# Optimization experiments

Measured on AMD Instinct MI355X. Metric: run time of the kernel, lower is better.

Reference implementation:

```python
import jax, jax.numpy as jnp
import numpy as np

NEG_SLOPE = 0.2

def _gat_layer(x, src, dst, W, a_src, a_dst, bias, concat):
    # x: [N, F_in]; W: [F_in, H*C]; a_src/a_dst: [H, C]; bias: [H*C] or [C]
    N = x.shape[0]
    H, C = a_src.shape
    h = (x @ W).reshape(N, H, C)                      # node features per head
    e_src = jnp.einsum('nhc,hc->nh', h, a_src)        # [N, H]
    e_dst = jnp.einsum('nhc,hc->nh', h, a_dst)        # [N, H]
    e = jax.nn.leaky_relu(e_src[src] + e_dst[dst], NEG_SLOPE)  # [E, H]
    # segment softmax over incoming edges of each destination node
    m = jax.ops.segment_max(e, dst, num_segments=N)   # [N, H]
    p = jnp.exp(e - m[dst])
    denom = jax.ops.segment_sum(p, dst, num_segments=N)
    alpha = p / denom[dst]                            # [E, H]
    msg = h[src] * alpha[:, :, None]                  # [E, H, C]
    out = jax.ops.segment_sum(msg, dst, num_segments=N)  # [N, H, C]
    if concat:
        out = out.reshape(N, H * C) + bias
    else:
        out = out.mean(axis=1) + bias
    return out, alpha


def setup_inputs() -> dict:
    key = jax.random.key(0)
    ks = jax.random.split(key, 12)
    N, E = 20000, 320000
    F_in, Ch, Co, H = 256, 64, 64, 8
    x = jax.random.normal(ks[0], (N, F_in), dtype=jnp.float32)
    edge_index = jax.random.randint(ks[1], (2, E), 0, N, dtype=jnp.int64)
    s = 0.05
    return {
        'x': x,
        'edge_index': edge_index,
        'W1': jax.random.normal(ks[2], (F_in, H * Ch), dtype=jnp.float32) * s,
        'att_src1': jax.random.normal(ks[3], (H, Ch), dtype=jnp.float32) * s,
        'att_dst1': jax.random.normal(ks[4], (H, Ch), dtype=jnp.float32) * s,
        'b1': jnp.zeros((H * Ch,), dtype=jnp.float32),
        'W2': jax.random.normal(ks[5], (H * Ch, H * Co), dtype=jnp.float32) * s,
        'att_src2': jax.random.normal(ks[6], (H, Co), dtype=jnp.float32) * s,
        'att_dst2': jax.random.normal(ks[7], (H, Co), dtype=jnp.float32) * s,
        'b2': jnp.zeros((Co,), dtype=jnp.float32),
    }


def reference(x, edge_index, W1, att_src1, att_dst1, b1, W2, att_src2, att_dst2, b2):
    N = x.shape[0]
    # PyG GATConv adds self-loops by default
    loop = jnp.arange(N, dtype=edge_index.dtype)
    src = jnp.concatenate([edge_index[0], loop])
    dst = jnp.concatenate([edge_index[1], loop])
    h1, alpha1 = _gat_layer(x, src, dst, W1, att_src1, att_dst1, b1, concat=True)
    h1 = jax.nn.relu(h1)
    h2, alpha2 = _gat_layer(h1, src, dst, W2, att_src2, att_dst2, b2, concat=False)
    return h2, alpha1, alpha2
```

## Files before the change

kernel.cpp:

```cpp
#include <hip/hip_runtime.h>

#define H 8
#define C 64
#define HC 512
#define NEG 0.2f

typedef __attribute__((ext_vector_type(8))) _Float16 half8v;
typedef __attribute__((ext_vector_type(4))) _Float16 half4v;
typedef __attribute__((ext_vector_type(4))) float f32x4;

__device__ __forceinline__ float leaky(float x) { return x > 0.f ? x : NEG * x; }

#define GLOAD_LDS16(gp, lp) \
  __builtin_amdgcn_global_load_lds((const __attribute__((address_space(1))) unsigned int*)(gp), \
                                   (__attribute__((address_space(3))) unsigned int*)(lp), 16, 0, 0)

__global__ void k_degree(const int* __restrict__ ei, int E, int N, int* __restrict__ deg) {
    int e = blockIdx.x * blockDim.x + threadIdx.x;
    int Et = E + N;
    if (e >= Et) return;
    int d = (e < E) ? ei[E + e] : (e - E);
    atomicAdd(&deg[d], 1);
}

__global__ __launch_bounds__(1024) void k_scan(const int* __restrict__ deg, int N, int* __restrict__ row_start) {
    __shared__ int part[1024];
    int t = threadIdx.x;
    int chunk = (N + 1023) >> 10;
    int lo = t * chunk, hi = min(lo + chunk, N);
    int s = 0;
    for (int i = lo; i < hi; ++i) s += deg[i];
    part[t] = s;
    __syncthreads();
    for (int off = 1; off < 1024; off <<= 1) {
        int v = (t >= off) ? part[t - off] : 0;
        __syncthreads();
        part[t] += v;
        __syncthreads();
    }
    int base = (t == 0) ? 0 : part[t - 1];
    for (int i = lo; i < hi; ++i) { row_start[i] = base; base += deg[i]; }
    if (t == 1023) row_start[N] = part[1023];
}

__global__ void k_fill(const int* __restrict__ ei, int E, int N,
                       const int* __restrict__ row_start, int* __restrict__ cursor,
                       int* __restrict__ csr_src, int* __restrict__ csr_eid,
                       int* __restrict__ csr_dst) {
    int e = blockIdx.x * blockDim.x + threadIdx.x;
    int Et = E + N;
    if (e >= Et) return;
    int d, s;
    if (e < E) { s = ei[e]; d = ei[E + e]; } else { s = e - E; d = s; }
    int pos = atomicAdd(&cursor[d], 1);
    int idx = row_start[d] + pos;
    csr_src[idx] = s;
    csr_eid[idx] = e;
    csr_dst[idx] = d;
}

__global__ void k_tofp16(const float* __restrict__ in, _Float16* __restrict__ out, int n4) {
    int i = blockIdx.x * blockDim.x + threadIdx.x;
    if (i >= n4) return;
    float4 v = reinterpret_cast<const float4*>(in)[i];
    half4v h;
    h[0] = (_Float16)v.x; h[1] = (_Float16)v.y;
    h[2] = (_Float16)v.z; h[3] = (_Float16)v.w;
    reinterpret_cast<half4v*>(out)[i] = h;
}

__global__ void k_tsplit(const float* __restrict__ W, _Float16* __restrict__ th,
                         _Float16* __restrict__ tl, int K, int Nc) {
    int idx = blockIdx.x * blockDim.x + threadIdx.x;
    if (idx >= K * Nc) return;
    int c = idx / K, k = idx - c * K;
    float v = W[(long)k * Nc + c];
    _Float16 hh = (_Float16)v;
    th[idx] = hh;
    tl[idx] = (_Float16)(v - (float)hh);
}

__global__ __launch_bounds__(256) void k_gemm_mfma(const _Float16* __restrict__ A,
                                                   const _Float16* __restrict__ Bh,
                                                   const _Float16* __restrict__ Bl,
                                                   _Float16* __restrict__ Cc, int M, int K, int Pb, int Mpad) {
    __shared__ _Float16 lA[8192], lBh[8192], lBl[8192];
    int bid = blockIdx.x;
    int panel = ((bid >> 5) << 3) + (bid & 7);
    int colb  = (bid >> 3) & 3;
    if (panel >= Pb) return;
    int tid = threadIdx.x;
    int w = tid >> 6, lane = tid & 63;
    int wr = w >> 1, wc = w & 1;
    int r0 = panel * 128, c0 = colb * 128;
    f32x4 acc[4][4] = {};
    int frag_off = ((lane >> 4) * 16 + (lane & 15)) * 8;

    int rb0 = tid >> 6, kc0 = (tid >> 4) & 3, r16_0 = tid & 15;
    int rb1 = (256 + tid) >> 6, kc1 = ((256 + tid) >> 4) & 3;
    long gaBase0 = (long)(r0 + rb0 * 16 + r16_0) * K + kc0 * 8;
    long gbBase0 = (long)(c0 + rb0 * 16 + r16_0) * K + kc0 * 8;
    long gaBase1 = (long)(r0 + rb1 * 16 + r16_0) * K + kc1 * 8;
    long gbBase1 = (long)(c0 + rb1 * 16 + r16_0) * K + kc1 * 8;
    int ldst0 = (w * 64) * 8;
    int ldst1 = (256 + w * 64) * 8;

#define STAGE(buf, k0)  do { \
        int off = (buf) * 4096; \
        GLOAD_LDS16(A  + gaBase0 + (k0), lA  + off + ldst0); \
        GLOAD_LDS16(Bh + gbBase0 + (k0), lBh + off + ldst0); \
        GLOAD_LDS16(Bl + gbBase0 + (k0), lBl + off + ldst0); \
        GLOAD_LDS16(A  + gaBase1 + (k0), lA  + off + ldst1); \
        GLOAD_LDS16(Bh + gbBase1 + (k0), lBh + off + ldst1); \
        GLOAD_LDS16(Bl + gbBase1 + (k0), lBl + off + ldst1); \
    } while (0)

    int nk = K >> 5;
    STAGE(0, 0);
    __syncthreads();
    int cur = 0;
    for (int t = 0; t < nk; ++t) {
        if (t + 1 < nk) STAGE(cur ^ 1, (t + 1) * 32);
        int off = cur * 4096;
        half8v fa[4], fbh[4], fbl[4];
        #pragma unroll
        for (int m = 0; m < 4; ++m) {
            int sa = off + (wr * 4 + m) * 512 + frag_off;
            fa[m] = *reinterpret_cast<half8v*>(&lA[sa]);
            int sb = off + (wc * 4 + m) * 512 + frag_off;
            fbh[m] = *reinterpret_cast<half8v*>(&lBh[sb]);
            fbl[m] = *reinterpret_cast<half8v*>(&lBl[sb]);
        }
        #pragma unroll
        for (int m = 0; m < 4; ++m)
            #pragma unroll
            for (int n = 0; n < 4; ++n) {
                acc[m][n] = __builtin_amdgcn_mfma_f32_16x16x32_f16(fa[m], fbh[n], acc[m][n], 0, 0, 0);
                acc[m][n] = __builtin_amdgcn_mfma_f32_16x16x32_f16(fa[m], fbl[n], acc[m][n], 0, 0, 0);
            }
        __syncthreads();
        cur ^= 1;
    }
#undef STAGE

    int head = colb * 2 + wc;
    long hbase = (long)head * Mpad * 64;
    #pragma unroll
    for (int m = 0; m < 4; ++m)
        #pragma unroll
        for (int j = 0; j < 4; ++j) {
            int gr = r0 + wr * 64 + m * 16 + (lane >> 4) * 4 + j;
            if (gr < M) {
                #pragma unroll
                for (int n = 0; n < 4; ++n)
                    Cc[hbase + (long)gr * 64 + n * 16 + (lane & 15)] = (_Float16)acc[m][n][j];
            }
        }
}

__global__ __launch_bounds__(512) void k_edot(const half8v* __restrict__ hp8,
                                              const float* __restrict__ a_src,
                                              const float* __restrict__ a_dst,
                                              float* __restrict__ e_src, float* __restrict__ e_dst,
                                              int N, int Mpad) {
    int h = threadIdx.x >> 6, lane = threadIdx.x & 63;
    int n8 = lane >> 3, cg = lane & 7;
    int n = blockIdx.x * 8 + n8;
    bool valid = (n < N);
    int nc = valid ? n : (N - 1);
    float as[8], ad[8];
    #pragma unroll
    for (int k = 0; k < 8; ++k) {
        as[k] = a_src[h * 64 + cg * 8 + k];
        ad[k] = a_dst[h * 64 + cg * 8 + k];
    }
    half8v hv = hp8[(long)h * Mpad * 8 + (long)nc * 8 + cg];
    float es = 0.f, ed = 0.f;
    #pragma unroll
    for (int k = 0; k < 8; ++k) {
        es = fmaf((float)hv[k], as[k], es);
        ed = fmaf((float)hv[k], ad[k], ed);
    }
    #pragma unroll
    for (int o = 1; o <= 4; o <<= 1) {
        es += __shfl_xor(es, o);
        ed += __shfl_xor(ed, o);
    }
    if (valid && cg == 0) {
        e_src[n * 8 + h] = es;
        e_dst[n * 8 + h] = ed;
    }
}

__global__ __launch_bounds__(512) void k_edge(const float* __restrict__ e_src,
                                              const float* __restrict__ e_dst,
                                              const int* __restrict__ row_start,
                                              const int* __restrict__ csr_src,
                                              float* __restrict__ alp_csr,
                                              float* __restrict__ inv_buf,
                                              int N) {
    int wid = threadIdx.x >> 6, lane = threadIdx.x & 63;
    int g = lane >> 5;
    int eg = (lane >> 3) & 3;
    int h = lane & 7;
    int n = blockIdx.x * 16 + wid * 2 + g;
    bool valid = (n < N);
    int nc = valid ? n : (N - 1);
    int row = row_start[nc];
    int deg = row_start[nc + 1] - row;
    float ed = e_dst[nc * 8 + h];
    int it = (deg + 3) >> 2;
    int itmax = max(it, __shfl_xor(it, 32));
    float psum = 0.f;
    for (int c = 0; c < itmax; ++c) {
        int e0 = c * 4 + eg;
        int idx = row + min(e0, deg - 1);
        int s = csr_src[idx];
        float p = (e0 < deg) ? __expf(leaky(e_src[s * 8 + h] + ed)) : 0.f;
        psum += p;
        if (valid && e0 < deg)
            alp_csr[(long)idx * 8 + h] = p;
    }
    psum += __shfl_xor(psum, 8);
    psum += __shfl_xor(psum, 16);
    float inv = 1.0f / psum;
    if (valid && eg == 0) inv_buf[n * 8 + h] = inv;
}

__global__ void k_alpha(const int* __restrict__ csr_dst, const int* __restrict__ csr_eid,
                        const float* __restrict__ alp_csr, const float* __restrict__ inv_buf,
                        float* __restrict__ alpha, int Et) {
    int idx = blockIdx.x * blockDim.x + threadIdx.x;
    if (idx >= Et) return;
    int d = csr_dst[idx], eid = csr_eid[idx];
    const float4* p4 = reinterpret_cast<const float4*>(alp_csr) + (long)idx * 2;
    const float4* i4 = reinterpret_cast<const float4*>(inv_buf) + (long)d * 2;
    float4 p0 = p4[0], p1 = p4[1], i0 = i4[0], i1 = i4[1];
    float4 r0, r1;
    r0.x = p0.x * i0.x; r0.y = p0.y * i0.y; r0.z = p0.z * i0.z; r0.w = p0.w * i0.w;
    r1.x = p1.x * i1.x; r1.y = p1.y * i1.y; r1.z = p1.z * i1.z; r1.w = p1.w * i1.w;
    float4* o4 = reinterpret_cast<float4*>(alpha) + (long)eid * 2;
    o4[0] = r0;
    o4[1] = r1;
}

__global__ __launch_bounds__(512) void k_gather(const half8v* __restrict__ hp8,
                                                const int* __restrict__ row_start,
                                                const int* __restrict__ csr_src,
                                                const float* __restrict__ alp_csr,
                                                const float* __restrict__ inv_buf,
                                                const float* __restrict__ bias,
                                                _Float16* __restrict__ h1,
                                                _Float16* __restrict__ accq,
                                                int N, int Mpad, int concat) {
    int wid = threadIdx.x >> 6, lane = threadIdx.x & 63;
    int bid = blockIdx.x;
    int h = bid & 7;
    int g = lane >> 5;
    int eg = (lane >> 3) & 3;
    int cg = lane & 7;
    int n = (bid >> 3) * 16 + wid * 2 + g;
    bool valid = (n < N);
    int nc = valid ? n : (N - 1);
    long hoff = (long)h * Mpad * 8;
    int row = row_start[nc];
    int deg = row_start[nc + 1] - row;
    float inv = inv_buf[nc * 8 + h];
    int it = (deg + 7) >> 3;
    int itmax = max(it, __shfl_xor(it, 32));
    float acc[8] = {};
    int idxA = row + min(eg, deg - 1);
    int idxB = row + min(4 + eg, deg - 1);
    int   sA = csr_src[idxA];
    float aA = alp_csr[(long)idxA * 8 + h];
    int   sB = csr_src[idxB];
    float aB = alp_csr[(long)idxB * 8 + h];
    for (int c = 0; c < itmax; ++c) {
        int e0 = c * 8 + eg, e1 = e0 + 4;
        int sA_c = sA, sB_c = sB;
        float aA_c = (e0 < deg) ? aA : 0.f;
        float aB_c = (e1 < deg) ? aB : 0.f;
        if (c + 1 < itmax) {
            int nA = row + min(e0 + 8, deg - 1);
            int nB = row + min(e1 + 8, deg - 1);
            sA = csr_src[nA];
            aA = alp_csr[(long)nA * 8 + h];
            sB = csr_src[nB];
            aB = alp_csr[(long)nB * 8 + h];
        }
        half8v hA = hp8[hoff + (long)sA_c * 8 + cg];
        half8v hB = hp8[hoff + (long)sB_c * 8 + cg];
        #pragma unroll
        for (int k = 0; k < 8; ++k) {
            acc[k] = fmaf((float)hA[k], aA_c, acc[k]);
            acc[k] = fmaf((float)hB[k], aB_c, acc[k]);
        }
    }
    #pragma unroll
    for (int o = 8; o <= 16; o <<= 1)
        #pragma unroll
        for (int k = 0; k < 8; ++k)
            acc[k] += __shfl_xor(acc[k], o);
    if (!valid) return;
    if (eg == 0) {
        if (concat) {
            half8v hh;
            #pragma unroll
            for (int k = 0; k < 8; ++k) {
                float v = fmaf(acc[k], inv, bias[h * 64 + cg * 8 + k]);
                v = v > 0.f ? v : 0.f;
                hh[k] = (_Float16)v;
            }
            reinterpret_cast<half8v*>(h1)[(long)n * 64 + h * 8 + cg] = hh;
        } else {
            half8v hv2;
            #pragma unroll
            for (int k = 0; k < 8; ++k) hv2[k] = (_Float16)(acc[k] * inv);
            reinterpret_cast<half8v*>(accq)[hoff + (long)n * 8 + cg] = hv2;
        }
    }
}

__global__ void k_mean(const _Float16* __restrict__ accq, const float* __restrict__ bias,
                       float* __restrict__ out, int N, int Mpad) {
    int i = blockIdx.x * blockDim.x + threadIdx.x;
    if (i >= N * 8) return;
    int n = i >> 3, cg = i & 7;
    float s[8] = {};
    #pragma unroll
    for (int h = 0; h < 8; ++h) {
        half8v v = reinterpret_cast<const half8v*>(accq)[(long)h * Mpad * 8 + (long)n * 8 + cg];
        #pragma unroll
        for (int k = 0; k < 8; ++k) s[k] += (float)v[k];
    }
    float4 r0, r1;
    r0.x = s[0] * 0.125f + bias[cg * 8 + 0];
    r0.y = s[1] * 0.125f + bias[cg * 8 + 1];
    r0.z = s[2] * 0.125f + bias[cg * 8 + 2];
    r0.w = s[3] * 0.125f + bias[cg * 8 + 3];
    r1.x = s[4] * 0.125f + bias[cg * 8 + 4];
    r1.y = s[5] * 0.125f + bias[cg * 8 + 5];
    r1.z = s[6] * 0.125f + bias[cg * 8 + 6];
    r1.w = s[7] * 0.125f + bias[cg * 8 + 7];
    float4* o4 = reinterpret_cast<float4*>(out + (long)n * 64 + cg * 8);
    o4[0] = r0;
    o4[1] = r1;
}

extern "C" void kernel_launch(void* const* d_in, const int* in_sizes, int n_in,
                              void* d_out, int out_size, void* d_ws, size_t ws_size,
                              hipStream_t stream) {
    const float* x   = (const float*)d_in[0];
    const int*   ei  = (const int*)d_in[1];
    const float* W1  = (const float*)d_in[2];
    const float* as1 = (const float*)d_in[3];
    const float* ad1 = (const float*)d_in[4];
    const float* b1  = (const float*)d_in[5];
    const float* W2  = (const float*)d_in[6];
    const float* as2 = (const float*)d_in[7];
    const float* ad2 = (const float*)d_in[8];
    const float* b2  = (const float*)d_in[9];

    int N  = in_sizes[0] / 256;
    int E  = in_sizes[1] / 2;
    int Et = E + N;
    int K1 = 256;
    int Mb   = (N + 127) / 128;
    int Mpad = Mb * 128;

    float* out    = (float*)d_out;
    float* h2_out = out;
    float* alpha1 = out + (size_t)N * 64;
    float* alpha2 = alpha1 + (size_t)Et * H;

    _Float16* hpre = (_Float16*)d_ws;
    _Float16* h1   = hpre + (size_t)Mpad * HC;
    _Float16* accq = h1 + (size_t)Mpad * HC;
    _Float16* xh   = accq + (size_t)Mpad * HC;
    _Float16* W1th = xh + (size_t)Mpad * K1;
    _Float16* W1tl = W1th + (size_t)HC * K1;
    _Float16* W2th = W1tl + (size_t)HC * K1;
    _Float16* W2tl = W2th + (size_t)HC * HC;
    float* eS     = (float*)(W2tl + (size_t)HC * HC);
    float* eD     = eS + (size_t)N * H;
    float* alpcsr = eD + (size_t)N * H;
    float* invb   = alpcsr + (size_t)Et * H;
    int*   deg    = (int*)(invb + (size_t)N * H);
    int*   cursor = deg + N;
    int*   row_st = cursor + N;
    int*   csr_src= row_st + N + 1;
    int*   csr_eid= csr_src + Et;
    int*   csr_dst= csr_eid + Et;

    hipMemsetAsync(deg, 0, (size_t)2 * N * sizeof(int), stream);
    int tb = 256;
    k_degree<<<(Et + tb - 1) / tb, tb, 0, stream>>>(ei, E, N, deg);
    k_scan<<<1, 1024, 0, stream>>>(deg, N, row_st);
    k_fill<<<(Et + tb - 1) / tb, tb, 0, stream>>>(ei, E, N, row_st, cursor, csr_src, csr_eid, csr_dst);

    int n4 = N * K1 / 4;
    k_tofp16<<<(n4 + tb - 1) / tb, tb, 0, stream>>>(x, xh, n4);
    k_tsplit<<<(K1 * HC + tb - 1) / tb, tb, 0, stream>>>(W1, W1th, W1tl, K1, HC);
    k_tsplit<<<(HC * HC + tb - 1) / tb, tb, 0, stream>>>(W2, W2th, W2tl, HC, HC);

    int Pb8 = ((Mb + 7) / 8) * 8;
    int ggemm = Pb8 * 4;
    int gedot = (N + 7) / 8;
    int gedge = (N + 15) / 16;
    int ggath = ((N + 15) / 16) * 8;
    k_gemm_mfma<<<ggemm, 256, 0, stream>>>(xh, W1th, W1tl, hpre, N, K1, Mb, Mpad);
    k_edot<<<gedot, 512, 0, stream>>>((const half8v*)hpre, as1, ad1, eS, eD, N, Mpad);
    k_edge<<<gedge, 512, 0, stream>>>(eS, eD, row_st, csr_src, alpcsr, invb, N);
    k_alpha<<<(Et + tb - 1) / tb, tb, 0, stream>>>(csr_dst, csr_eid, alpcsr, invb, alpha1, Et);
    k_gather<<<ggath, 512, 0, stream>>>((const half8v*)hpre, row_st, csr_src, alpcsr, invb,
                                        b1, h1, nullptr, N, Mpad, 1);
    k_gemm_mfma<<<ggemm, 256, 0, stream>>>(h1, W2th, W2tl, hpre, N, HC, Mb, Mpad);
    k_edot<<<gedot, 512, 0, stream>>>((const half8v*)hpre, as2, ad2, eS, eD, N, Mpad);
    k_edge<<<gedge, 512, 0, stream>>>(eS, eD, row_st, csr_src, alpcsr, invb, N);
    k_alpha<<<(Et + tb - 1) / tb, tb, 0, stream>>>(csr_dst, csr_eid, alpcsr, invb, alpha2, Et);
    k_gather<<<ggath, 512, 0, stream>>>((const half8v*)hpre, row_st, csr_src, alpcsr, invb,
                                        b2, nullptr, accq, N, Mpad, 0);
    k_mean<<<(N * 8 + tb - 1) / tb, tb, 0, stream>>>(accq, b2, h2_out, N, Mpad);
}
```

Baseline: 280.5 us.

## Drop split-fp16 weight GEMM and store head-major packed (src, p) edge pairs

The weight matrices are now cast to a single fp16 copy instead of a hi/lo split, which halves the B-operand loads and the MFMA count in both GEMMs. This gives up the extra weight precision the lo term provided. The edge kernel now writes head-major int2 (source, unnormalized p) pairs plus a head-major inverse-sum copy. The gather can then fetch each edge's source index and weight in one contiguous load per head instead of strided loads from csr_src and an [E,8] buffer. k_alpha now reads eight strided int2 entries per edge, so the alpha output pass may get more expensive.

```diff
diff --git a/kernel.cpp b/kernel.cpp
--- a/kernel.cpp
+++ b/kernel.cpp
@@ -69,22 +69,17 @@
     reinterpret_cast<half4v*>(out)[i] = h;
 }
 
-__global__ void k_tsplit(const float* __restrict__ W, _Float16* __restrict__ th,
-                         _Float16* __restrict__ tl, int K, int Nc) {
+__global__ void k_tcast(const float* __restrict__ W, _Float16* __restrict__ th, int K, int Nc) {
     int idx = blockIdx.x * blockDim.x + threadIdx.x;
     if (idx >= K * Nc) return;
     int c = idx / K, k = idx - c * K;
-    float v = W[(long)k * Nc + c];
-    _Float16 hh = (_Float16)v;
-    th[idx] = hh;
-    tl[idx] = (_Float16)(v - (float)hh);
+    th[idx] = (_Float16)W[(long)k * Nc + c];
 }
 
 __global__ __launch_bounds__(256) void k_gemm_mfma(const _Float16* __restrict__ A,
-                                                   const _Float16* __restrict__ Bh,
-                                                   const _Float16* __restrict__ Bl,
+                                                   const _Float16* __restrict__ B,
                                                    _Float16* __restrict__ Cc, int M, int K, int Pb, int Mpad) {
-    __shared__ _Float16 lA[8192], lBh[8192], lBl[8192];
+    __shared__ _Float16 lA[8192], lB[8192];
     int bid = blockIdx.x;
     int panel = ((bid >> 5) << 3) + (bid & 7);
     int colb  = (bid >> 3) & 3;
@@ -107,12 +102,10 @@
 
 #define STAGE(buf, k0)  do { \
         int off = (buf) * 4096; \
-        GLOAD_LDS16(A  + gaBase0 + (k0), lA  + off + ldst0); \
-        GLOAD_LDS16(Bh + gbBase0 + (k0), lBh + off + ldst0); \
-        GLOAD_LDS16(Bl + gbBase0 + (k0), lBl + off + ldst0); \
-        GLOAD_LDS16(A  + gaBase1 + (k0), lA  + off + ldst1); \
-        GLOAD_LDS16(Bh + gbBase1 + (k0), lBh + off + ldst1); \
-        GLOAD_LDS16(Bl + gbBase1 + (k0), lBl + off + ldst1); \
+        GLOAD_LDS16(A + gaBase0 + (k0), lA + off + ldst0); \
+        GLOAD_LDS16(B + gbBase0 + (k0), lB + off + ldst0); \
+        GLOAD_LDS16(A + gaBase1 + (k0), lA + off + ldst1); \
+        GLOAD_LDS16(B + gbBase1 + (k0), lB + off + ldst1); \
     } while (0)
 
     int nk = K >> 5;
@@ -122,22 +115,19 @@
     for (int t = 0; t < nk; ++t) {
         if (t + 1 < nk) STAGE(cur ^ 1, (t + 1) * 32);
         int off = cur * 4096;
-        half8v fa[4], fbh[4], fbl[4];
+        half8v fa[4], fb[4];
         #pragma unroll
         for (int m = 0; m < 4; ++m) {
             int sa = off + (wr * 4 + m) * 512 + frag_off;
             fa[m] = *reinterpret_cast<half8v*>(&lA[sa]);
             int sb = off + (wc * 4 + m) * 512 + frag_off;
-            fbh[m] = *reinterpret_cast<half8v*>(&lBh[sb]);
-            fbl[m] = *reinterpret_cast<half8v*>(&lBl[sb]);
+            fb[m] = *reinterpret_cast<half8v*>(&lB[sb]);
         }
         #pragma unroll
         for (int m = 0; m < 4; ++m)
             #pragma unroll
-            for (int n = 0; n < 4; ++n) {
-                acc[m][n] = __builtin_amdgcn_mfma_f32_16x16x32_f16(fa[m], fbh[n], acc[m][n], 0, 0, 0);
-                acc[m][n] = __builtin_amdgcn_mfma_f32_16x16x32_f16(fa[m], fbl[n], acc[m][n], 0, 0, 0);
-            }
+            for (int n = 0; n < 4; ++n)
+                acc[m][n] = __builtin_amdgcn_mfma_f32_16x16x32_f16(fa[m], fb[n], acc[m][n], 0, 0, 0);
         __syncthreads();
         cur ^= 1;
     }
@@ -196,9 +186,10 @@
                                               const float* __restrict__ e_dst,
                                               const int* __restrict__ row_start,
                                               const int* __restrict__ csr_src,
-                                              float* __restrict__ alp_csr,
-                                              float* __restrict__ inv_buf,
-                                              int N) {
+                                              int2* __restrict__ sp,
+                                              float* __restrict__ inv_nm,
+                                              float* __restrict__ inv_hm,
+                                              int N, int Et) {
     int wid = threadIdx.x >> 6, lane = threadIdx.x & 63;
     int g = lane >> 5;
     int eg = (lane >> 3) & 3;
@@ -209,6 +200,7 @@
     int row = row_start[nc];
     int deg = row_start[nc + 1] - row;
     float ed = e_dst[nc * 8 + h];
+    long hEt = (long)h * Et;
     int it = (deg + 3) >> 2;
     int itmax = max(it, __shfl_xor(it, 32));
     float psum = 0.f;
@@ -219,40 +211,43 @@
         float p = (e0 < deg) ? __expf(leaky(e_src[s * 8 + h] + ed)) : 0.f;
         psum += p;
         if (valid && e0 < deg)
-            alp_csr[(long)idx * 8 + h] = p;
+            sp[hEt + idx] = make_int2(s, __float_as_int(p));
     }
     psum += __shfl_xor(psum, 8);
     psum += __shfl_xor(psum, 16);
     float inv = 1.0f / psum;
-    if (valid && eg == 0) inv_buf[n * 8 + h] = inv;
+    if (valid && eg == 0) {
+        inv_nm[n * 8 + h] = inv;
+        inv_hm[h * N + n] = inv;
+    }
 }
 
 __global__ void k_alpha(const int* __restrict__ csr_dst, const int* __restrict__ csr_eid,
-                        const float* __restrict__ alp_csr, const float* __restrict__ inv_buf,
+                        const int2* __restrict__ sp, const float* __restrict__ inv_nm,
                         float* __restrict__ alpha, int Et) {
     int idx = blockIdx.x * blockDim.x + threadIdx.x;
     if (idx >= Et) return;
     int d = csr_dst[idx], eid = csr_eid[idx];
-    const float4* p4 = reinterpret_cast<const float4*>(alp_csr) + (long)idx * 2;
-    const float4* i4 = reinterpret_cast<const float4*>(inv_buf) + (long)d * 2;
-    float4 p0 = p4[0], p1 = p4[1], i0 = i4[0], i1 = i4[1];
-    float4 r0, r1;
-    r0.x = p0.x * i0.x; r0.y = p0.y * i0.y; r0.z = p0.z * i0.z; r0.w = p0.w * i0.w;
-    r1.x = p1.x * i1.x; r1.y = p1.y * i1.y; r1.z = p1.z * i1.z; r1.w = p1.w * i1.w;
+    const float4* i4 = reinterpret_cast<const float4*>(inv_nm) + (long)d * 2;
+    float4 i0 = i4[0], i1 = i4[1];
+    float iv[8] = {i0.x, i0.y, i0.z, i0.w, i1.x, i1.y, i1.z, i1.w};
+    float r[8];
+    #pragma unroll
+    for (int h = 0; h < 8; ++h)
+        r[h] = __int_as_float(sp[(long)h * Et + idx].y) * iv[h];
     float4* o4 = reinterpret_cast<float4*>(alpha) + (long)eid * 2;
-    o4[0] = r0;
-    o4[1] = r1;
+    o4[0] = make_float4(r[0], r[1], r[2], r[3]);
+    o4[1] = make_float4(r[4], r[5], r[6], r[7]);
 }
 
 __global__ __launch_bounds__(512) void k_gather(const half8v* __restrict__ hp8,
                                                 const int* __restrict__ row_start,
-                                                const int* __restrict__ csr_src,
-                                                const float* __restrict__ alp_csr,
-                                                const float* __restrict__ inv_buf,
+                                                const int2* __restrict__ sp,
+                                                const float* __restrict__ inv_hm,
                                                 const float* __restrict__ bias,
                                                 _Float16* __restrict__ h1,
                                                 _Float16* __restrict__ accq,
-                                                int N, int Mpad, int concat) {
+                                                int N, int Mpad, int Et, int concat) {
     int wid = threadIdx.x >> 6, lane = threadIdx.x & 63;
     int bid = blockIdx.x;
     int h = bid & 7;
@@ -263,37 +258,29 @@
     bool valid = (n < N);
     int nc = valid ? n : (N - 1);
     long hoff = (long)h * Mpad * 8;
+    const int2* sph = sp + (long)h * Et;
     int row = row_start[nc];
     int deg = row_start[nc + 1] - row;
-    float inv = inv_buf[nc * 8 + h];
     int it = (deg + 7) >> 3;
     int itmax = max(it, __shfl_xor(it, 32));
     float acc[8] = {};
-    int idxA = row + min(eg, deg - 1);
-    int idxB = row + min(4 + eg, deg - 1);
-    int   sA = csr_src[idxA];
-    float aA = alp_csr[(long)idxA * 8 + h];
-    int   sB = csr_src[idxB];
-    float aB = alp_csr[(long)idxB * 8 + h];
+    int2 pA = sph[row + min(eg, deg - 1)];
+    int2 pB = sph[row + min(4 + eg, deg - 1)];
     for (int c = 0; c < itmax; ++c) {
         int e0 = c * 8 + eg, e1 = e0 + 4;
-        int sA_c = sA, sB_c = sB;
-        float aA_c = (e0 < deg) ? aA : 0.f;
-        float aB_c = (e1 < deg) ? aB : 0.f;
+        int   sA = pA.x, sB = pB.x;
+        float aA = (e0 < deg) ? __int_as_float(pA.y) : 0.f;
+        float aB = (e1 < deg) ? __int_as_float(pB.y) : 0.f;
         if (c + 1 < itmax) {
-            int nA = row + min(e0 + 8, deg - 1);
-            int nB = row + min(e1 + 8, deg - 1);
-            sA = csr_src[nA];
-            aA = alp_csr[(long)nA * 8 + h];
-            sB = csr_src[nB];
-            aB = alp_csr[(long)nB * 8 + h];
+            pA = sph[row + min(e0 + 8, deg - 1)];
+            pB = sph[row + min(e1 + 8, deg - 1)];
         }
-        half8v hA = hp8[hoff + (long)sA_c * 8 + cg];
-        half8v hB = hp8[hoff + (long)sB_c * 8 + cg];
+        half8v hA = hp8[hoff + (long)sA * 8 + cg];
+        half8v hB = hp8[hoff + (long)sB * 8 + cg];
         #pragma unroll
         for (int k = 0; k < 8; ++k) {
-            acc[k] = fmaf((float)hA[k], aA_c, acc[k]);
-            acc[k] = fmaf((float)hB[k], aB_c, acc[k]);
+            acc[k] = fmaf((float)hA[k], aA, acc[k]);
+            acc[k] = fmaf((float)hB[k], aB, acc[k]);
         }
     }
     #pragma unroll
@@ -302,6 +289,7 @@
         for (int k = 0; k < 8; ++k)
             acc[k] += __shfl_xor(acc[k], o);
     if (!valid) return;
+    float inv = inv_hm[h * N + n];
     if (eg == 0) {
         if (concat) {
             half8v hh;
@@ -377,15 +365,14 @@
     _Float16* h1   = hpre + (size_t)Mpad * HC;
     _Float16* accq = h1 + (size_t)Mpad * HC;
     _Float16* xh   = accq + (size_t)Mpad * HC;
-    _Float16* W1th = xh + (size_t)Mpad * K1;
-    _Float16* W1tl = W1th + (size_t)HC * K1;
-    _Float16* W2th = W1tl + (size_t)HC * K1;
-    _Float16* W2tl = W2th + (size_t)HC * HC;
-    float* eS     = (float*)(W2tl + (size_t)HC * HC);
+    _Float16* W1t  = xh + (size_t)Mpad * K1;
+    _Float16* W2t  = W1t + (size_t)HC * K1;
+    float* eS     = (float*)(W2t + (size_t)HC * HC);
     float* eD     = eS + (size_t)N * H;
-    float* alpcsr = eD + (size_t)N * H;
-    float* invb   = alpcsr + (size_t)Et * H;
-    int*   deg    = (int*)(invb + (size_t)N * H);
+    float* invnm  = eD + (size_t)N * H;
+    float* invhm  = invnm + (size_t)N * H;
+    int2* sp      = (int2*)(invhm + (size_t)N * H);
+    int*   deg    = (int*)(sp + (size_t)H * Et);
     int*   cursor = deg + N;
     int*   row_st = cursor + N;
     int*   csr_src= row_st + N + 1;
@@ -400,25 +387,25 @@
 
     int n4 = N * K1 / 4;
     k_tofp16<<<(n4 + tb - 1) / tb, tb, 0, stream>>>(x, xh, n4);
-    k_tsplit<<<(K1 * HC + tb - 1) / tb, tb, 0, stream>>>(W1, W1th, W1tl, K1, HC);
-    k_tsplit<<<(HC * HC + tb - 1) / tb, tb, 0, stream>>>(W2, W2th, W2tl, HC, HC);
+    k_tcast<<<(K1 * HC + tb - 1) / tb, tb, 0, stream>>>(W1, W1t, K1, HC);
+    k_tcast<<<(HC * HC + tb - 1) / tb, tb, 0, stream>>>(W2, W2t, HC, HC);
 
     int Pb8 = ((Mb + 7) / 8) * 8;
     int ggemm = Pb8 * 4;
     int gedot = (N + 7) / 8;
     int gedge = (N + 15) / 16;
     int ggath = ((N + 15) / 16) * 8;
-    k_gemm_mfma<<<ggemm, 256, 0, stream>>>(xh, W1th, W1tl, hpre, N, K1, Mb, Mpad);
+    k_gemm_mfma<<<ggemm, 256, 0, stream>>>(xh, W1t, hpre, N, K1, Mb, Mpad);
     k_edot<<<gedot, 512, 0, stream>>>((const half8v*)hpre, as1, ad1, eS, eD, N, Mpad);
-    k_edge<<<gedge, 512, 0, stream>>>(eS, eD, row_st, csr_src, alpcsr, invb, N);
-    k_alpha<<<(Et + tb - 1) / tb, tb, 0, stream>>>(csr_dst, csr_eid, alpcsr, invb, alpha1, Et);
-    k_gather<<<ggath, 512, 0, stream>>>((const half8v*)hpre, row_st, csr_src, alpcsr, invb,
-                                        b1, h1, nullptr, N, Mpad, 1);
-    k_gemm_mfma<<<ggemm, 256, 0, stream>>>(h1, W2th, W2tl, hpre, N, HC, Mb, Mpad);
+    k_edge<<<gedge, 512, 0, stream>>>(eS, eD, row_st, csr_src, sp, invnm, invhm, N, Et);
+    k_alpha<<<(Et + tb - 1) / tb, tb, 0, stream>>>(csr_dst, csr_eid, sp, invnm, alpha1, Et);
+    k_gather<<<ggath, 512, 0, stream>>>((const half8v*)hpre, row_st, sp, invhm,
+                                        b1, h1, nullptr, N, Mpad, Et, 1);
+    k_gemm_mfma<<<ggemm, 256, 0, stream>>>(h1, W2t, hpre, N, HC, Mb, Mpad);
     k_edot<<<gedot, 512, 0, stream>>>((const half8v*)hpre, as2, ad2, eS, eD, N, Mpad);
-    k_edge<<<gedge, 512, 0, stream>>>(eS, eD, row_st, csr_src, alpcsr, invb, N);
-    k_alpha<<<(Et + tb - 1) / tb, tb, 0, stream>>>(csr_dst, csr_eid, alpcsr, invb, alpha2, Et);
-    k_gather<<<ggath, 512, 0, stream>>>((const half8v*)hpre, row_st, csr_src, alpcsr, invb,
-                                        b2, nullptr, accq, N, Mpad, 0);
+    k_edge<<<gedge, 512, 0, stream>>>(eS, eD, row_st, csr_src, sp, invnm, invhm, N, Et);
+    k_alpha<<<(Et + tb - 1) / tb, tb, 0, stream>>>(csr_dst, csr_eid, sp, invnm, alpha2, Et);
+    k_gather<<<ggath, 512, 0, stream>>>((const half8v*)hpre, row_st, sp, invhm,
+                                        b2, nullptr, accq, N, Mpad, Et, 0);
     k_mean<<<(N * 8 + tb - 1) / tb, tb, 0, stream>>>(accq, b2, h2_out, N, Mpad);
 }
```

Result: no change. 282.2 us (+0.6%).
